# Optimization experiments

Measured on AMD Instinct MI355X. Metric: run time of the kernel, lower is better.

## Reference

```python
import jax, jax.numpy as jnp
import numpy as np

N = 100000      # nodes
E = 1600000     # directed edges (avg degree 16)
F_IN = 128
HID = 64
OUT = 10


def setup_inputs() -> dict:
    key = jax.random.key(0)
    ks = jax.random.split(key, 6)
    x = jax.random.normal(ks[0], (N, F_IN), dtype=jnp.float32)
    edge_index = jax.random.randint(ks[1], (2, E), 0, N, dtype=jnp.int32)
    # Glorot-scaled weights like PyG's GCNConv.lin; bias added post-aggregation
    W1 = jax.random.normal(ks[2], (F_IN, HID), dtype=jnp.float32) * np.float32(1.0 / np.sqrt(F_IN))
    b1 = jnp.zeros((HID,), dtype=jnp.float32)
    W2 = jax.random.normal(ks[3], (HID, OUT), dtype=jnp.float32) * np.float32(1.0 / np.sqrt(HID))
    b2 = jnp.zeros((OUT,), dtype=jnp.float32)
    return {"x": x, "edge_index": edge_index, "W1": W1, "b1": b1, "W2": W2, "b2": b2}


def _gcn_norm(edge_index, num_nodes):
    """Add self-loops and compute symmetric normalization D^-1/2 A D^-1/2 (PyG gcn_norm)."""
    loops = jnp.arange(num_nodes, dtype=edge_index.dtype)
    src = jnp.concatenate([edge_index[0], loops])
    dst = jnp.concatenate([edge_index[1], loops])
    deg = jax.ops.segment_sum(jnp.ones_like(dst, dtype=jnp.float32), dst, num_segments=num_nodes)
    dinv = jnp.where(deg > 0, jax.lax.rsqrt(deg), 0.0)  # inf -> 0 as in PyG
    norm = dinv[src] * dinv[dst]  # [E+N]
    return src, dst, norm


def _gcn_conv(x, src, dst, norm, W, b, num_nodes):
    h = x @ W                                   # transform first (smaller dim aggregated)
    msg = h[src] * norm[:, None]                # gather + scale
    agg = jax.ops.segment_sum(msg, dst, num_segments=num_nodes)  # scatter-add
    return agg + b


def reference(x, edge_index, W1, b1, W2, b2):
    src, dst, norm = _gcn_norm(edge_index, N)
    h = jax.nn.relu(_gcn_conv(x, src, dst, norm, W1, b1, N))
    # F.dropout(training=self.training): identity in eval mode
    out = _gcn_conv(h, src, dst, norm, W2, b2, N)
    return out
```

## Files before the change

### kernel.cpp

```cpp
#include <hip/hip_runtime.h>
#include <hip/hip_fp16.h>

static constexpr int F = 128;
static constexpr int H = 64;
static constexpr int O = 10;
static constexpr int PSU = 6;
static constexpr int NBUK_MAX = 256;
static constexpr int CAP = 12288;
static constexpr int ESCAP = 14336;
static constexpr int EPB = 4096;
static constexpr int XPAD = 136;

typedef _Float16 half8 __attribute__((ext_vector_type(8)));
typedef float floatx4 __attribute__((ext_vector_type(4)));

__global__ __launch_bounds__(256) void k_init(int* __restrict__ bcntg,
                                              const float* __restrict__ W1,
                                              __half* __restrict__ W1f,
                                              unsigned* __restrict__ yN,
                                              unsigned* __restrict__ zsN) {
    int b = blockIdx.x, t = threadIdx.x;
    if (b == 0) {
        bcntg[t] = 0;
        if (t < 32) yN[t] = 0u;
        if (t < PSU) zsN[t] = 0u;
    } else {
        int i = (b - 1) * 256 + t;
        int j = i & 7, lane = (i >> 3) & 63, sc = i >> 9;
        int s = sc >> 2, c = sc & 3;
        int k = s * 32 + (lane >> 4) * 8 + j;
        int nn = c * 16 + (lane & 15);
        W1f[i] = __float2half(W1[k * H + nn]);
    }
}

__global__ __launch_bounds__(256) void k_bin(const int* __restrict__ src,
                                             const int* __restrict__ dst,
                                             int* __restrict__ bcntg,
                                             unsigned* __restrict__ ebuf, int e_total) {
    __shared__ int hist[NBUK_MAX];
    __shared__ int base[NBUK_MAX];
    __shared__ int loc[NBUK_MAX];
    int t = threadIdx.x;
    hist[t] = 0;
    loc[t] = 0;
    __syncthreads();
    int i0 = blockIdx.x * EPB;
    int i1 = min(i0 + EPB, e_total);
    int i = i0 + 4 * t;
    for (; i + 3 < i1; i += 1024) {
        int4 d4 = *(const int4*)&dst[i];
        atomicAdd(&hist[d4.x >> 9], 1);
        atomicAdd(&hist[d4.y >> 9], 1);
        atomicAdd(&hist[d4.z >> 9], 1);
        atomicAdd(&hist[d4.w >> 9], 1);
    }
    for (; i < i1; ++i) atomicAdd(&hist[dst[i] >> 9], 1);
    __syncthreads();
    if (hist[t] > 0) base[t] = atomicAdd(&bcntg[t], hist[t]);
    __syncthreads();
    i = i0 + 4 * t;
    for (; i + 3 < i1; i += 1024) {
        int4 s4 = *(const int4*)&src[i];
        int4 d4 = *(const int4*)&dst[i];
#pragma unroll
        for (int u = 0; u < 4; ++u) {
            int s = (&s4.x)[u], d = (&d4.x)[u];
            int b = d >> 9;
            int r = base[b] + atomicAdd(&loc[b], 1);
            if (r < CAP)
                ebuf[(size_t)b * CAP + r] = ((unsigned)(d & 511) << 17) | (unsigned)s;
        }
    }
    for (; i < i1; ++i) {
        int s = src[i], d = dst[i];
        int b = d >> 9;
        int r = base[b] + atomicAdd(&loc[b], 1);
        if (r < CAP)
            ebuf[(size_t)b * CAP + r] = ((unsigned)(d & 511) << 17) | (unsigned)s;
    }
}

__global__ __launch_bounds__(256) void k_bsort(
    const unsigned* __restrict__ ebuf, const int* __restrict__ bcntg,
    int* __restrict__ rowbeg, int* __restrict__ degp, float* __restrict__ dinv,
    int* __restrict__ esrc, int n_nodes) {
    __shared__ int hc[512];
    __shared__ int sa[512];
    __shared__ int sb[512];
    int t = threadIdx.x, b = blockIdx.x, n0 = b << 9;
    hc[t] = 0;
    hc[t + 256] = 0;
    __syncthreads();
    int cb = min(bcntg[b], CAP);
    const unsigned* eb = ebuf + (size_t)b * CAP;
    int i = 4 * t;
    for (; i + 3 < cb; i += 1024) {
        uint4 e4 = *(const uint4*)&eb[i];
        atomicAdd(&hc[e4.x >> 17], 1);
        atomicAdd(&hc[e4.y >> 17], 1);
        atomicAdd(&hc[e4.z >> 17], 1);
        atomicAdd(&hc[e4.w >> 17], 1);
    }
    for (; i < cb; ++i) atomicAdd(&hc[eb[i] >> 17], 1);
    __syncthreads();
#pragma unroll
    for (int u = 0; u < 2; ++u) {
        int ii = t + 256 * u;
        sa[ii] = (hc[ii] + 15) & ~15;
    }
    __syncthreads();
    int* A = sa;
    int* Bp = sb;
    for (int off = 1; off < 512; off <<= 1) {
#pragma unroll
        for (int u = 0; u < 2; ++u) {
            int ii = t + 256 * u;
            int v = A[ii];
            if (ii >= off) v += A[ii - off];
            Bp[ii] = v;
        }
        __syncthreads();
        int* tmp = A; A = Bp; Bp = tmp;
    }
#pragma unroll
    for (int u = 0; u < 2; ++u) {
        int ii = t + 256 * u;
        int cnt = hc[ii];
        int cp = (cnt + 15) & ~15;
        int excl = A[ii] - cp;
        Bp[ii] = excl;
        int n = n0 + ii;
        if (n < n_nodes) {
            rowbeg[n] = b * ESCAP + excl;
            degp[n] = cp;
            dinv[n] = rsqrtf((float)cnt + 1.0f);
        }
    }
    __syncthreads();
    int* es = esrc + (size_t)b * ESCAP;
    i = 4 * t;
    for (; i + 3 < cb; i += 1024) {
        uint4 e4 = *(const uint4*)&eb[i];
#pragma unroll
        for (int u = 0; u < 4; ++u) {
            unsigned e = (&e4.x)[u];
            int r = atomicAdd(&Bp[e >> 17], 1);
            es[r] = (int)(e & 0x1FFFFu);
        }
    }
    for (; i < cb; ++i) {
        unsigned e = eb[i];
        int r = atomicAdd(&Bp[e >> 17], 1);
        es[r] = (int)(e & 0x1FFFFu);
    }
    __syncthreads();
#pragma unroll
    for (int u = 0; u < 2; ++u) {
        int ii = t + 256 * u;
        int end = A[ii];
        for (int p = Bp[ii]; p < end; ++p) es[p] = n_nodes;
    }
}

__global__ __launch_bounds__(256, 4) void k_gemm1(
    const float* __restrict__ x, const __half* __restrict__ W1f,
    const float* __restrict__ dinv, __half* __restrict__ y, int n_nodes) {
    __shared__ __half xh[64 * XPAD];
    const int tid = threadIdx.x;
    const int lane = tid & 63;
    const int w = tid >> 6;
    const int row0 = blockIdx.x * 64;

    half8 bf[16];
    const uint4* wf = (const uint4*)W1f;
#pragma unroll
    for (int sc = 0; sc < 16; ++sc) {
        union { uint4 u; half8 h; } tmp;
        tmp.u = wf[sc * 64 + lane];
        bf[sc] = tmp.h;
    }

    for (int i = tid; i < 64 * 32; i += 256) {
        int r = i >> 5, k4 = i & 31;
        int gr = row0 + r;
        if (gr < n_nodes) {
            float4 v = *(const float4*)&x[(size_t)gr * F + 4 * k4];
            __half2 p0 = __floats2half2_rn(v.x, v.y);
            __half2 p1 = __floats2half2_rn(v.z, v.w);
            uint2 pk = make_uint2(*(unsigned*)&p0, *(unsigned*)&p1);
            *(uint2*)&xh[r * XPAD + 4 * k4] = pk;
        }
    }
    __syncthreads();

    const int m16 = lane & 15, quad = lane >> 4;
    floatx4 acc[4];
#pragma unroll
    for (int c = 0; c < 4; ++c) acc[c] = (floatx4){0.f, 0.f, 0.f, 0.f};
#pragma unroll
    for (int s = 0; s < 4; ++s) {
        union { uint4 u; half8 h; } ua;
        ua.u = *(const uint4*)&xh[(16 * w + m16) * XPAD + s * 32 + quad * 8];
#pragma unroll
        for (int c = 0; c < 4; ++c)
            acc[c] = __builtin_amdgcn_mfma_f32_16x16x32_f16(ua.h, bf[s * 4 + c],
                                                            acc[c], 0, 0, 0);
    }
#pragma unroll
    for (int r = 0; r < 4; ++r) {
        int grow = row0 + 16 * w + quad * 4 + r;
        if (grow < n_nodes) {
            float d = dinv[grow];
#pragma unroll
            for (int c = 0; c < 4; ++c)
                y[(size_t)grow * H + c * 16 + m16] = __float2half(acc[c][r] * d);
        }
    }
}

__global__ __launch_bounds__(256) void k_gather1z(
    const uint2* __restrict__ yq, const int* __restrict__ rowbeg,
    const int* __restrict__ degp, const int* __restrict__ esrc,
    const float* __restrict__ dinv, const float* __restrict__ b1,
    const float* __restrict__ W2, unsigned* __restrict__ zs_u, int n_nodes) {
    __shared__ float w2s[H * O];
    for (int i = threadIdx.x; i < H * O; i += 256) w2s[i] = W2[i];
    __syncthreads();
    const int l = threadIdx.x & 63;
    const int g = l >> 4;
    const int c = l & 15;
    const int n = blockIdx.x * 4 + (threadIdx.x >> 6);
    if (n >= n_nodes) return;
    const int beg = rowbeg[n];
    const int dp = degp[n];
    const int idx = esrc[beg + l];
    float2 aA = make_float2(0.f, 0.f);
    float2 aB = make_float2(0.f, 0.f);
    if (g == 0) {
        uint2 v = yq[(size_t)n * 16 + c];
        float2 fA = __half22float2(*(const __half2*)&v.x);
        float2 fB = __half22float2(*(const __half2*)&v.y);
        aA.x += fA.x; aA.y += fA.y; aB.x += fB.x; aB.y += fB.y;
    }
    const int dlim = min(dp, 64);
    for (int k = 0; k < dlim; k += 16) {
#pragma unroll
        for (int u = 0; u < 4; ++u) {
            int s = __shfl(idx, k + 4 * u + g, 64);
            uint2 v = yq[(size_t)s * 16 + c];
            float2 fA = __half22float2(*(const __half2*)&v.x);
            float2 fB = __half22float2(*(const __half2*)&v.y);
            aA.x += fA.x; aA.y += fA.y; aB.x += fB.x; aB.y += fB.y;
        }
    }
    for (int kk = 64; kk < dp; kk += 4) {
        int s = esrc[beg + kk + g];
        uint2 v = yq[(size_t)s * 16 + c];
        float2 fA = __half22float2(*(const __half2*)&v.x);
        float2 fB = __half22float2(*(const __half2*)&v.y);
        aA.x += fA.x; aA.y += fA.y; aB.x += fB.x; aB.y += fB.y;
    }
#pragma unroll
    for (int off = 16; off <= 32; off <<= 1) {
        aA.x += __shfl_xor(aA.x, off, 64);
        aA.y += __shfl_xor(aA.y, off, 64);
        aB.x += __shfl_xor(aB.x, off, 64);
        aB.y += __shfl_xor(aB.y, off, 64);
    }
    const float4 bb = ((const float4*)b1)[c];
    const float d = dinv[n];
    const float h0 = fmaxf(fmaf(d, aA.x, bb.x), 0.0f);
    const float h1 = fmaxf(fmaf(d, aA.y, bb.y), 0.0f);
    const float h2 = fmaxf(fmaf(d, aB.x, bb.z), 0.0f);
    const float h3 = fmaxf(fmaf(d, aB.y, bb.w), 0.0f);
    const float* wr = &w2s[(4 * c) * O];
    const int ja = 2 * g;
    float sa0 = h0 * wr[0 * O + ja]     + h1 * wr[1 * O + ja]
              + h2 * wr[2 * O + ja]     + h3 * wr[3 * O + ja];
    float sa1 = h0 * wr[0 * O + ja + 1] + h1 * wr[1 * O + ja + 1]
              + h2 * wr[2 * O + ja + 1] + h3 * wr[3 * O + ja + 1];
    float sb0 = h0 * wr[0 * O + 8]      + h1 * wr[1 * O + 8]
              + h2 * wr[2 * O + 8]      + h3 * wr[3 * O + 8];
    float sb1 = h0 * wr[0 * O + 9]      + h1 * wr[1 * O + 9]
              + h2 * wr[2 * O + 9]      + h3 * wr[3 * O + 9];
#pragma unroll
    for (int m = 1; m <= 8; m <<= 1) {
        sa0 += __shfl_xor(sa0, m, 64);
        sa1 += __shfl_xor(sa1, m, 64);
        sb0 += __shfl_xor(sb0, m, 64);
        sb1 += __shfl_xor(sb1, m, 64);
    }
    const size_t rb = (size_t)n * PSU;
    if (c == 0) {
        __half2 pa = __floats2half2_rn(sa0 * d, sa1 * d);
        zs_u[rb + g] = *(const unsigned*)&pa;
    }
    if (l == 1) {
        __half2 pb = __floats2half2_rn(sb0 * d, sb1 * d);
        zs_u[rb + 4] = *(const unsigned*)&pb;
    }
    if (l == 2) zs_u[rb + 5] = 0u;
}

__global__ __launch_bounds__(256) void k_gather2(
    const unsigned* __restrict__ zs_u, const int* __restrict__ rowbeg,
    const int* __restrict__ degp, const int* __restrict__ esrc,
    const float* __restrict__ dinv, const float* __restrict__ b2,
    float* __restrict__ out, int n_nodes) {
    const int l = threadIdx.x & 63;
    const int j = l & 7;
    const int sbase = l & ~7;
    const int jj = (j < 5) ? j : 5;
    const int n = blockIdx.x * 32 + (threadIdx.x >> 3);
    if (n >= n_nodes) return;
    const int beg = rowbeg[n];
    const int dp = degp[n];
    unsigned v0 = zs_u[(size_t)n * PSU + jj];
    float2 acc = __half22float2(*(const __half2*)&v0);
    for (int k0 = 0; k0 < dp; k0 += 8) {
        int idx = esrc[beg + k0 + j];
#pragma unroll
        for (int e = 0; e < 8; ++e) {
            int s = __shfl(idx, sbase + e, 64);
            unsigned v = zs_u[(size_t)s * PSU + jj];
            float2 f = __half22float2(*(const __half2*)&v);
            acc.x += f.x;
            acc.y += f.y;
        }
    }
    if (j < 5) {
        float2 bb = ((const float2*)b2)[j];
        float d = dinv[n];
        float2 o = make_float2(fmaf(d, acc.x, bb.x), fmaf(d, acc.y, bb.y));
        *(float2*)&out[(size_t)n * O + 2 * j] = o;
    }
}

static inline size_t align256(size_t v) { return (v + 255) & ~(size_t)255; }

extern "C" void kernel_launch(void* const* d_in, const int* in_sizes, int n_in,
                              void* d_out, int out_size, void* d_ws, size_t ws_size,
                              hipStream_t stream) {
    const float* x  = (const float*)d_in[0];
    const int*   ei = (const int*)d_in[1];
    const float* W1 = (const float*)d_in[2];
    const float* b1 = (const float*)d_in[3];
    const float* W2 = (const float*)d_in[4];
    const float* b2 = (const float*)d_in[5];
    float* out = (float*)d_out;

    const int N = in_sizes[0] / F;
    const int E = in_sizes[1] / 2;
    const int* src = ei;
    const int* dst = ei + E;
    const int NBUK = (N + 511) >> 9;

    char* base = (char*)d_ws;
    __half* y = (__half*)base;
    size_t ysz = align256((size_t)(N + 1) * H * 2);
    char* hreg = base + ysz;
    unsigned* ebuf = (unsigned*)hreg;
    __half* W1f = (__half*)(hreg + (size_t)N * H * 2 - (size_t)F * H * 2);
    size_t hsz = align256((size_t)N * H * 2);
    char* zreg = hreg + hsz;
    unsigned* zs_u = (unsigned*)zreg;
    size_t zsz = align256((size_t)(N + 1) * PSU * 4);
    float* dinv = (float*)(zreg + zsz);
    int* rowbeg = (int*)(dinv + N);
    int* degp = rowbeg + N;
    int* bcntg = degp + N;
    int* esrc = bcntg + 256;

    const int nb_bin = (E + EPB - 1) / EPB;

    k_init<<<1 + F * H / 256, 256, 0, stream>>>(bcntg, W1, W1f,
                                                (unsigned*)(y + (size_t)N * H),
                                                zs_u + (size_t)N * PSU);
    k_bin<<<nb_bin, 256, 0, stream>>>(src, dst, bcntg, ebuf, E);
    k_bsort<<<NBUK, 256, 0, stream>>>(ebuf, bcntg, rowbeg, degp, dinv, esrc, N);
    k_gemm1<<<(N + 63) / 64, 256, 0, stream>>>(x, W1f, dinv, y, N);
    k_gather1z<<<(N + 3) / 4, 256, 0, stream>>>((const uint2*)y, rowbeg, degp,
                                                esrc, dinv, b1, W2, zs_u, N);
    k_gather2<<<(N + 31) / 32, 256, 0, stream>>>(zs_u, rowbeg, degp, esrc,
                                                 dinv, b2, out, N);
}
```

Baseline: 218.8 us.

## Remap layer-1 gather to eight lanes per node with 16-byte row loads

Result: faster. 189.9 us (-13.2%).

```diff
diff --git a/kernel.cpp b/kernel.cpp
--- a/kernel.cpp
+++ b/kernel.cpp
@@ -220,87 +220,82 @@
 }
 
 __global__ __launch_bounds__(256) void k_gather1z(
-    const uint2* __restrict__ yq, const int* __restrict__ rowbeg,
+    const uint4* __restrict__ yq4, const int* __restrict__ rowbeg,
     const int* __restrict__ degp, const int* __restrict__ esrc,
     const float* __restrict__ dinv, const float* __restrict__ b1,
     const float* __restrict__ W2, unsigned* __restrict__ zs_u, int n_nodes) {
-    __shared__ float w2s[H * O];
-    for (int i = threadIdx.x; i < H * O; i += 256) w2s[i] = W2[i];
+    __shared__ float w2t[O * H];
+    for (int i = threadIdx.x; i < O * H; i += 256)
+        w2t[i] = W2[(i & 63) * O + (i >> 6)];
     __syncthreads();
     const int l = threadIdx.x & 63;
-    const int g = l >> 4;
-    const int c = l & 15;
-    const int n = blockIdx.x * 4 + (threadIdx.x >> 6);
+    const int c = l & 7;
+    const int gbase = l & ~7;
+    const int n = blockIdx.x * 32 + (threadIdx.x >> 3);
     if (n >= n_nodes) return;
     const int beg = rowbeg[n];
     const int dp = degp[n];
-    const int idx = esrc[beg + l];
-    float2 aA = make_float2(0.f, 0.f);
-    float2 aB = make_float2(0.f, 0.f);
-    if (g == 0) {
-        uint2 v = yq[(size_t)n * 16 + c];
-        float2 fA = __half22float2(*(const __half2*)&v.x);
-        float2 fB = __half22float2(*(const __half2*)&v.y);
-        aA.x += fA.x; aA.y += fA.y; aB.x += fB.x; aB.y += fB.y;
-    }
-    const int dlim = min(dp, 64);
-    for (int k = 0; k < dlim; k += 16) {
-#pragma unroll
-        for (int u = 0; u < 4; ++u) {
-            int s = __shfl(idx, k + 4 * u + g, 64);
-            uint2 v = yq[(size_t)s * 16 + c];
-            float2 fA = __half22float2(*(const __half2*)&v.x);
-            float2 fB = __half22float2(*(const __half2*)&v.y);
-            aA.x += fA.x; aA.y += fA.y; aB.x += fB.x; aB.y += fB.y;
-        }
-    }
-    for (int kk = 64; kk < dp; kk += 4) {
-        int s = esrc[beg + kk + g];
-        uint2 v = yq[(size_t)s * 16 + c];
-        float2 fA = __half22float2(*(const __half2*)&v.x);
-        float2 fB = __half22float2(*(const __half2*)&v.y);
-        aA.x += fA.x; aA.y += fA.y; aB.x += fB.x; aB.y += fB.y;
-    }
-#pragma unroll
-    for (int off = 16; off <= 32; off <<= 1) {
-        aA.x += __shfl_xor(aA.x, off, 64);
-        aA.y += __shfl_xor(aA.y, off, 64);
-        aB.x += __shfl_xor(aB.x, off, 64);
-        aB.y += __shfl_xor(aB.y, off, 64);
-    }
-    const float4 bb = ((const float4*)b1)[c];
     const float d = dinv[n];
-    const float h0 = fmaxf(fmaf(d, aA.x, bb.x), 0.0f);
-    const float h1 = fmaxf(fmaf(d, aA.y, bb.y), 0.0f);
-    const float h2 = fmaxf(fmaf(d, aB.x, bb.z), 0.0f);
-    const float h3 = fmaxf(fmaf(d, aB.y, bb.w), 0.0f);
-    const float* wr = &w2s[(4 * c) * O];
-    const int ja = 2 * g;
-    float sa0 = h0 * wr[0 * O + ja]     + h1 * wr[1 * O + ja]
-              + h2 * wr[2 * O + ja]     + h3 * wr[3 * O + ja];
-    float sa1 = h0 * wr[0 * O + ja + 1] + h1 * wr[1 * O + ja + 1]
-              + h2 * wr[2 * O + ja + 1] + h3 * wr[3 * O + ja + 1];
-    float sb0 = h0 * wr[0 * O + 8]      + h1 * wr[1 * O + 8]
-              + h2 * wr[2 * O + 8]      + h3 * wr[3 * O + 8];
-    float sb1 = h0 * wr[0 * O + 9]      + h1 * wr[1 * O + 9]
-              + h2 * wr[2 * O + 9]      + h3 * wr[3 * O + 9];
-#pragma unroll
-    for (int m = 1; m <= 8; m <<= 1) {
-        sa0 += __shfl_xor(sa0, m, 64);
-        sa1 += __shfl_xor(sa1, m, 64);
-        sb0 += __shfl_xor(sb0, m, 64);
-        sb1 += __shfl_xor(sb1, m, 64);
-    }
-    const size_t rb = (size_t)n * PSU;
+
+    float acc[8];
+    {
+        uint4 v = yq4[(size_t)n * 8 + c];
+        float2 f0 = __half22float2(*(const __half2*)&v.x);
+        float2 f1 = __half22float2(*(const __half2*)&v.y);
+        float2 f2 = __half22float2(*(const __half2*)&v.z);
+        float2 f3 = __half22float2(*(const __half2*)&v.w);
+        acc[0] = f0.x; acc[1] = f0.y; acc[2] = f1.x; acc[3] = f1.y;
+        acc[4] = f2.x; acc[5] = f2.y; acc[6] = f3.x; acc[7] = f3.y;
+    }
+    for (int k0 = 0; k0 < dp; k0 += 16) {
+        int2 idx = *(const int2*)&esrc[beg + k0 + 2 * c];
+#pragma unroll
+        for (int e = 0; e < 16; ++e) {
+            int s = __shfl((e & 1) ? idx.y : idx.x, gbase + (e >> 1), 64);
+            uint4 v = yq4[(size_t)s * 8 + c];
+            float2 f0 = __half22float2(*(const __half2*)&v.x);
+            float2 f1 = __half22float2(*(const __half2*)&v.y);
+            float2 f2 = __half22float2(*(const __half2*)&v.z);
+            float2 f3 = __half22float2(*(const __half2*)&v.w);
+            acc[0] += f0.x; acc[1] += f0.y; acc[2] += f1.x; acc[3] += f1.y;
+            acc[4] += f2.x; acc[5] += f2.y; acc[6] += f3.x; acc[7] += f3.y;
+        }
+    }
+    const float4 ba = ((const float4*)b1)[2 * c];
+    const float4 bbv = ((const float4*)b1)[2 * c + 1];
+    float h[8];
+    h[0] = fmaxf(fmaf(d, acc[0], ba.x), 0.0f);
+    h[1] = fmaxf(fmaf(d, acc[1], ba.y), 0.0f);
+    h[2] = fmaxf(fmaf(d, acc[2], ba.z), 0.0f);
+    h[3] = fmaxf(fmaf(d, acc[3], ba.w), 0.0f);
+    h[4] = fmaxf(fmaf(d, acc[4], bbv.x), 0.0f);
+    h[5] = fmaxf(fmaf(d, acc[5], bbv.y), 0.0f);
+    h[6] = fmaxf(fmaf(d, acc[6], bbv.z), 0.0f);
+    h[7] = fmaxf(fmaf(d, acc[7], bbv.w), 0.0f);
+    float p[O];
+#pragma unroll
+    for (int j = 0; j < O; ++j) {
+        float4 wa = *(const float4*)&w2t[j * 64 + 8 * c];
+        float4 wb = *(const float4*)&w2t[j * 64 + 8 * c + 4];
+        p[j] = h[0] * wa.x + h[1] * wa.y + h[2] * wa.z + h[3] * wa.w
+             + h[4] * wb.x + h[5] * wb.y + h[6] * wb.z + h[7] * wb.w;
+    }
+#pragma unroll
+    for (int m = 1; m <= 4; m <<= 1) {
+#pragma unroll
+        for (int j = 0; j < O; ++j) p[j] += __shfl_xor(p[j], m, 64);
+    }
     if (c == 0) {
-        __half2 pa = __floats2half2_rn(sa0 * d, sa1 * d);
-        zs_u[rb + g] = *(const unsigned*)&pa;
-    }
-    if (l == 1) {
-        __half2 pb = __floats2half2_rn(sb0 * d, sb1 * d);
-        zs_u[rb + 4] = *(const unsigned*)&pb;
-    }
-    if (l == 2) zs_u[rb + 5] = 0u;
+        __half2 q0 = __floats2half2_rn(p[0] * d, p[1] * d);
+        __half2 q1 = __floats2half2_rn(p[2] * d, p[3] * d);
+        __half2 q2 = __floats2half2_rn(p[4] * d, p[5] * d);
+        __half2 q3 = __floats2half2_rn(p[6] * d, p[7] * d);
+        __half2 q4 = __floats2half2_rn(p[8] * d, p[9] * d);
+        uint2* zp = (uint2*)&zs_u[(size_t)n * PSU];
+        zp[0] = make_uint2(*(const unsigned*)&q0, *(const unsigned*)&q1);
+        zp[1] = make_uint2(*(const unsigned*)&q2, *(const unsigned*)&q3);
+        zp[2] = make_uint2(*(const unsigned*)&q4, 0u);
+    }
 }
 
 __global__ __launch_bounds__(256) void k_gather2(
@@ -380,8 +375,8 @@
     k_bin<<<nb_bin, 256, 0, stream>>>(src, dst, bcntg, ebuf, E);
     k_bsort<<<NBUK, 256, 0, stream>>>(ebuf, bcntg, rowbeg, degp, dinv, esrc, N);
     k_gemm1<<<(N + 63) / 64, 256, 0, stream>>>(x, W1f, dinv, y, N);
-    k_gather1z<<<(N + 3) / 4, 256, 0, stream>>>((const uint2*)y, rowbeg, degp,
-                                                esrc, dinv, b1, W2, zs_u, N);
+    k_gather1z<<<(N + 31) / 32, 256, 0, stream>>>((const uint4*)y, rowbeg, degp,
+                                                  esrc, dinv, b1, W2, zs_u, N);
     k_gather2<<<(N + 31) / 32, 256, 0, stream>>>(zs_u, rowbeg, degp, esrc,
                                                  dinv, b2, out, N);
 }
```
